# Optimization experiments

Measured on AMD Instinct MI355X. Metric: run time of the kernel, lower is better.

## Reference

```python
import math
import jax, jax.numpy as jnp
import numpy as np

B, S, D, H = 4, 2048, 1024, 16
DK = D // H


def setup_inputs() -> dict:
    key = jax.random.key(0)
    ks = jax.random.split(key, 12)
    scale = 1.0 / math.sqrt(D)
    inp = {
        "query": jax.random.normal(ks[0], (B, S, D), jnp.float32),
        "key": jax.random.normal(ks[1], (B, S, D), jnp.float32),
        "value": jax.random.normal(ks[2], (B, S, D), jnp.float32),
        # causal mask, broadcasts over batch and (after unsqueeze) heads
        "mask": jnp.tril(jnp.ones((1, S, S), jnp.int32)),
        # torch Linear weights: [out_features, in_features]
        "Wq": jax.random.uniform(ks[3], (D, D), jnp.float32, -scale, scale),
        "bq": jax.random.uniform(ks[4], (D,), jnp.float32, -scale, scale),
        "Wk": jax.random.uniform(ks[5], (D, D), jnp.float32, -scale, scale),
        "bk": jax.random.uniform(ks[6], (D,), jnp.float32, -scale, scale),
        "Wv": jax.random.uniform(ks[7], (D, D), jnp.float32, -scale, scale),
        "bv": jax.random.uniform(ks[8], (D,), jnp.float32, -scale, scale),
        "Wo": jax.random.uniform(ks[9], (D, D), jnp.float32, -scale, scale),
        "bo": jax.random.uniform(ks[10], (D,), jnp.float32, -scale, scale),
    }
    return inp


def _proj(x, W, b):
    # torch Linear: x @ W.T + b, then split heads -> [B, H, S, DK]
    y = jnp.einsum('bsd,ed->bse', x, W) + b
    return y.reshape(x.shape[0], x.shape[1], H, DK).transpose(0, 2, 1, 3)


def reference(query, key, value, mask, Wq, bq, Wk, bk, Wv, bv, Wo, bo):
    q = _proj(query, Wq, bq)
    k = _proj(key, Wk, bk)
    v = _proj(value, Wv, bv)
    # scores: [B, H, S, S]
    scores = jnp.einsum('bhqd,bhkd->bhqk', q, k) / math.sqrt(DK)
    m = mask[:, None, :, :]  # mask.unsqueeze(1) -> broadcast over heads
    scores = jnp.where(m == 0, jnp.float32(-1e9), scores)
    prob = jax.nn.softmax(scores, axis=-1)
    # dropout is identity in eval mode
    x = jnp.einsum('bhqk,bhkd->bhqd', prob, v)
    x = x.transpose(0, 2, 1, 3).reshape(query.shape[0], -1, H * DK)
    return jnp.einsum('bsd,ed->bse', x, Wo) + bo
```

## Files before the change

### kernel.cpp

```cpp
#include <hip/hip_runtime.h>
#include <hip/hip_bf16.h>

#define DI __device__ __forceinline__

typedef __bf16 bf16x8 __attribute__((ext_vector_type(8)));
typedef unsigned short u16x8 __attribute__((ext_vector_type(8)));
typedef unsigned short u16x4 __attribute__((ext_vector_type(4)));
typedef unsigned int u32x4 __attribute__((ext_vector_type(4)));
typedef float f32x4 __attribute__((ext_vector_type(4)));
typedef float f32x16 __attribute__((ext_vector_type(16)));

constexpr int kB = 4, kS = 2048, kD = 1024, kH = 16;
constexpr int kM = kB * kS;

DI unsigned short f2bf(float f) {
  union { float f; unsigned u; } x; x.f = f;
  unsigned r = x.u + 0x7fffu + ((x.u >> 16) & 1u);
  return (unsigned short)(r >> 16);
}

DI f32x4 mfma16(u16x8 a, u16x8 b, f32x4 c) {
  return __builtin_amdgcn_mfma_f32_16x16x32_bf16(
      __builtin_bit_cast(bf16x8, a), __builtin_bit_cast(bf16x8, b), c, 0, 0, 0);
}
DI f32x16 mfma32(u16x8 a, u16x8 b, f32x16 c) {
  return __builtin_amdgcn_mfma_f32_32x32x16_bf16(
      __builtin_bit_cast(bf16x8, a), __builtin_bit_cast(bf16x8, b), c, 0, 0, 0);
}

DI void gload16(const unsigned short* g, unsigned short* l) {
  __builtin_amdgcn_global_load_lds(
      (__attribute__((address_space(1))) void*)g,
      (__attribute__((address_space(3))) void*)l, 16, 0, 0);
}

DI unsigned pkbf(float lo, float hi) {
  unsigned r;
  asm("v_cvt_pk_bf16_f32 %0, %1, %2" : "=v"(r) : "v"(lo), "v"(hi));
  return r;
}

__global__ __launch_bounds__(256) void conv_w(const float* __restrict__ s0,
                                              const float* __restrict__ s1,
                                              const float* __restrict__ s2,
                                              const float* __restrict__ s3,
                                              unsigned short* __restrict__ d) {
  const int j = blockIdx.y;
  const float* s = j == 0 ? s0 : j == 1 ? s1 : j == 2 ? s2 : s3;
  const size_t i = ((size_t)blockIdx.x * 256 + threadIdx.x) * 8;
  f32x4 a = *reinterpret_cast<const f32x4*>(s + i);
  f32x4 b = *reinterpret_cast<const f32x4*>(s + i + 4);
  u16x8 o;
#pragma unroll
  for (int jj = 0; jj < 4; ++jj) { o[jj] = f2bf(a[jj]); o[jj + 4] = f2bf(b[jj]); }
  *reinterpret_cast<u16x8*>(d + (size_t)j * 1048576 + i) = o;
}

__global__ __launch_bounds__(256) void proj_gemm(
    const float* __restrict__ A, const unsigned short* __restrict__ W,
    const float* __restrict__ bias, float scale, int vmode,
    unsigned short* __restrict__ O) {
  constexpr int K = kD, N = kD;
  __shared__ unsigned short As[128][64];
  __shared__ unsigned short Bs[2][128][64];

  const int lin = blockIdx.y * 8 + blockIdx.x;
  const int rm = (lin & 7) * 64 + (lin >> 3);
  const int n0 = (rm & 7) * 128, m0 = (rm >> 3) * 128;

  const int t = threadIdx.x;
  const int wave = t >> 6, lane = t & 63;
  const int wr = (wave >> 1) * 64, wc = (wave & 1) * 64;
  const int lrow = lane & 15, lkq = lane >> 4;

  const int rl = lane >> 3;
  const int bcs8 = ((lane & 7) ^ rl) * 8;
  const unsigned short* bsrc = W + ((size_t)(n0 + wave * 32 + rl)) * K + bcs8;
  unsigned short* bl = &Bs[0][0][0] + wave * 2048;

  const int ar_r = t >> 3, ar_c = t & 7;
  const int asw = (ar_c ^ (ar_r & 7)) * 8;
  const float* abase = A + (size_t)(m0 + ar_r) * K + ar_c * 8;

  f32x4 ar0[4], ar1[4];
#pragma unroll
  for (int i = 0; i < 4; ++i) {
    const float* ap = abase + (size_t)i * 32 * K;
    ar0[i] = *reinterpret_cast<const f32x4*>(ap);
    ar1[i] = *reinterpret_cast<const f32x4*>(ap + 4);
  }
#pragma unroll
  for (int i = 0; i < 4; ++i) gload16(bsrc + (size_t)i * 8 * K, bl + i * 512);

  f32x4 acc[4][4];
#pragma unroll
  for (int m = 0; m < 4; ++m)
#pragma unroll
    for (int n = 0; n < 4; ++n) acc[m][n] = f32x4{0.f, 0.f, 0.f, 0.f};

  for (int kt = 0; kt < K; kt += 64) {
    const int cb = (kt >> 6) & 1;
    __builtin_amdgcn_s_barrier();
#pragma unroll
    for (int i = 0; i < 4; ++i) {
      u32x4 w;
      w[0] = pkbf(ar0[i][0], ar0[i][1]);
      w[1] = pkbf(ar0[i][2], ar0[i][3]);
      w[2] = pkbf(ar1[i][0], ar1[i][1]);
      w[3] = pkbf(ar1[i][2], ar1[i][3]);
      *reinterpret_cast<u32x4*>(&As[ar_r + i * 32][asw]) = w;
    }
    asm volatile("s_waitcnt lgkmcnt(0)" ::: "memory");
    __builtin_amdgcn_s_barrier();

    if (kt + 64 < K) {
#pragma unroll
      for (int i = 0; i < 4; ++i)
        gload16(bsrc + (size_t)i * 8 * K + kt + 64, bl + (cb ^ 1) * 8192 + i * 512);
#pragma unroll
      for (int i = 0; i < 4; ++i) {
        const float* ap = abase + (size_t)i * 32 * K + kt + 64;
        ar0[i] = *reinterpret_cast<const f32x4*>(ap);
        ar1[i] = *reinterpret_cast<const f32x4*>(ap + 4);
      }
      asm volatile("s_waitcnt vmcnt(12)" ::: "memory");
    } else {
      asm volatile("s_waitcnt vmcnt(0)" ::: "memory");
    }

    u16x8 af[4][2], bf[4][2];
#pragma unroll
    for (int m = 0; m < 4; ++m) {
      const int row = wr + m * 16 + lrow;
#pragma unroll
      for (int kk = 0; kk < 2; ++kk)
        af[m][kk] = *reinterpret_cast<const u16x8*>(
            &As[row][((kk * 4 + lkq) ^ (row & 7)) * 8]);
    }
#pragma unroll
    for (int n = 0; n < 4; ++n) {
      const int row = wc + n * 16 + lrow;
#pragma unroll
      for (int kk = 0; kk < 2; ++kk)
        bf[n][kk] = *reinterpret_cast<const u16x8*>(
            &Bs[cb][row][((kk * 4 + lkq) ^ (row & 7)) * 8]);
    }
#pragma unroll
    for (int kk = 0; kk < 2; ++kk)
#pragma unroll
      for (int m = 0; m < 4; ++m)
#pragma unroll
        for (int n = 0; n < 4; ++n)
          acc[m][n] = mfma16(af[m][kk], bf[n][kk], acc[m][n]);
  }

#pragma unroll
  for (int n = 0; n < 4; ++n) {
    const int gc = n0 + wc + n * 16 + lrow;
    const float bvv = bias[gc];
#pragma unroll
    for (int m = 0; m < 4; ++m) {
      const int gr = m0 + wr + m * 16 + lkq * 4;
      if (vmode) {
        u16x4 o4;
#pragma unroll
        for (int j = 0; j < 4; ++j) o4[j] = f2bf(acc[m][n][j] + bvv);
        const size_t idx = ((size_t)(gr >> 11) * 1024 + gc) * 2048 + (gr & 2047);
        *reinterpret_cast<u16x4*>(O + idx) = o4;
      } else {
#pragma unroll
        for (int j = 0; j < 4; ++j)
          O[(size_t)(gr + j) * N + gc] = f2bf((acc[m][n][j] + bvv) * scale);
      }
    }
  }
}

__global__ __launch_bounds__(256) void gemm_o(const unsigned short* __restrict__ A,
                                              const unsigned short* __restrict__ W,
                                              const float* __restrict__ bias,
                                              float* __restrict__ C) {
  constexpr int K = kD, N = kD;
  __shared__ unsigned short As[2][128][64];
  __shared__ unsigned short Bs[2][128][64];

  const int lin = blockIdx.y * 8 + blockIdx.x;
  const int rm = (lin & 7) * 64 + (lin >> 3);
  const int n0 = (rm & 7) * 128, m0 = (rm >> 3) * 128;

  const int t = threadIdx.x;
  const int wave = t >> 6, lane = t & 63;
  const int wr = (wave >> 1) * 64, wc = (wave & 1) * 64;
  const int lrow = lane & 15, lkq = lane >> 4;

  const int rl = lane >> 3;
  const int cs8 = ((lane & 7) ^ rl) * 8;
  const unsigned short* asrc = A + ((size_t)(m0 + wave * 32 + rl)) * K + cs8;
  const unsigned short* bsrc = W + ((size_t)(n0 + wave * 32 + rl)) * K + cs8;

#define STAGEO(ii)                                                          \
  {                                                                         \
    const int i_ = (ii);                                                    \
    const int kt_ = i_ * 64;                                                \
    unsigned short* al_ = &As[i_ & 1][0][0] + wave * 2048;                  \
    unsigned short* bl_ = &Bs[i_ & 1][0][0] + wave * 2048;                  \
    _Pragma("unroll") for (int g_ = 0; g_ < 4; ++g_) {                      \
      gload16(asrc + (size_t)g_ * 8 * K + kt_, al_ + g_ * 512);             \
      gload16(bsrc + (size_t)g_ * 8 * K + kt_, bl_ + g_ * 512);             \
    }                                                                       \
  }

  STAGEO(0);

  f32x4 acc[4][4];
#pragma unroll
  for (int m = 0; m < 4; ++m)
#pragma unroll
    for (int n = 0; n < 4; ++n) acc[m][n] = f32x4{0.f, 0.f, 0.f, 0.f};

  for (int i = 0; i < 16; ++i) {
    __builtin_amdgcn_s_barrier();
    if (i + 1 < 16) {
      STAGEO(i + 1);
      asm volatile("s_waitcnt vmcnt(8)" ::: "memory");
    } else {
      asm volatile("s_waitcnt vmcnt(0)" ::: "memory");
    }
    const int cb = i & 1;
    u16x8 af[4][2], bf[4][2];
#pragma unroll
    for (int m = 0; m < 4; ++m) {
      const int row = wr + m * 16 + lrow;
#pragma unroll
      for (int kk = 0; kk < 2; ++kk)
        af[m][kk] = *reinterpret_cast<const u16x8*>(
            &As[cb][row][((kk * 4 + lkq) ^ (row & 7)) * 8]);
    }
#pragma unroll
    for (int n = 0; n < 4; ++n) {
      const int row = wc + n * 16 + lrow;
#pragma unroll
      for (int kk = 0; kk < 2; ++kk)
        bf[n][kk] = *reinterpret_cast<const u16x8*>(
            &Bs[cb][row][((kk * 4 + lkq) ^ (row & 7)) * 8]);
    }
#pragma unroll
    for (int kk = 0; kk < 2; ++kk)
#pragma unroll
      for (int m = 0; m < 4; ++m)
#pragma unroll
        for (int n = 0; n < 4; ++n)
          acc[m][n] = mfma16(af[m][kk], bf[n][kk], acc[m][n]);
  }
#undef STAGEO

#pragma unroll
  for (int n = 0; n < 4; ++n) {
    const int gc = n0 + wc + n * 16 + lrow;
    const float bvv = bias[gc];
#pragma unroll
    for (int m = 0; m < 4; ++m) {
      const int gr = m0 + wr + m * 16 + lkq * 4;
#pragma unroll
      for (int j = 0; j < 4; ++j)
        C[(size_t)(gr + j) * N + gc] = acc[m][n][j] + bvv;
    }
  }
}

__global__ __launch_bounds__(256) void attn_fused(
    const unsigned short* __restrict__ qb, const unsigned short* __restrict__ kb,
    const unsigned short* __restrict__ vbT, unsigned short* __restrict__ ob) {
  __shared__ unsigned short Ks[2][128][64];
  __shared__ unsigned short Vt[2][64][128];

  const int lin = blockIdx.y * 8 + blockIdx.x;
  const int rmap = (lin & 7) * 64 + (lin >> 3);
  const int bh = rmap >> 3;
  const int p = rmap & 7;
  const int b = bh >> 4, h = bh & 15;

  const int t = threadIdx.x;
  const int wave = t >> 6, lane = t & 63;
  const int lq = lane & 31, hi = lane >> 5;
  const int sw7 = lq & 7, sw15 = lq & 15;

  const int np0 = p + 1;
  constexpr int NT = 17;

  const int krl = lane >> 3;
  const int kcs = ((lane & 7) ^ krl) * 8;
  const unsigned short* kbase =
      kb + ((size_t)(b * kS) + wave * 32 + krl) * kD + h * 64 + kcs;
  const int vrl = lane >> 4, vc = lane & 15;
  const size_t vrow = (size_t)(bh * 64) + wave * 16 + vrl;
  const unsigned short* vsrc0 = vbT + (vrow + 0) * kS + (size_t)((vc ^ (vrl + 0)) * 8);
  const unsigned short* vsrc1 = vbT + (vrow + 4) * kS + (size_t)((vc ^ (vrl + 4)) * 8);
  const unsigned short* vsrc2 = vbT + (vrow + 8) * kS + (size_t)((vc ^ (vrl + 8)) * 8);
  const unsigned short* vsrc3 = vbT + (vrow + 12) * kS + (size_t)((vc ^ (vrl + 12)) * 8);

#define STAGE(ii)                                                  \
  {                                                                \
    const int i_ = (ii);                                           \
    const int kv_ = (i_ < np0 ? i_ : i_ - np0) * 128;              \
    unsigned short* kd_ = &Ks[i_ & 1][wave * 32][0];               \
    const unsigned short* kp_ = kbase + (size_t)kv_ * kD;          \
    gload16(kp_, kd_);                                             \
    gload16(kp_ + (size_t)8 * kD, kd_ + 512);                      \
    gload16(kp_ + (size_t)16 * kD, kd_ + 1024);                    \
    gload16(kp_ + (size_t)24 * kD, kd_ + 1536);                    \
    unsigned short* vd_ = &Vt[i_ & 1][wave * 16][0];               \
    gload16(vsrc0 + kv_, vd_);                                     \
    gload16(vsrc1 + kv_, vd_ + 512);                               \
    gload16(vsrc2 + kv_, vd_ + 1024);                              \
    gload16(vsrc3 + kv_, vd_ + 1536);                              \
  }

  int qt = p;
  int qw0 = qt * 128 + wave * 32;
  int qg = qw0 + lq;

  u16x8 bq[4];
  {
    const unsigned short* qrow = qb + ((size_t)(b * kS) + qg) * kD + h * 64;
#pragma unroll
    for (int s = 0; s < 4; ++s)
      bq[s] = *reinterpret_cast<const u16x8*>(qrow + s * 16 + hi * 8);
  }

  f32x16 oT0, oT1;
#pragma unroll
  for (int jj = 0; jj < 16; ++jj) { oT0[jj] = 0.f; oT1[jj] = 0.f; }
  float lsum = 0.f;

  STAGE(0);

  for (int i = 0; i < NT; ++i) {
    if (i == np0) {
      float ls = lsum + __shfl_xor(lsum, 32);
      const float rinv = 1.f / ls;
      unsigned short* orow = ob + ((size_t)(b * kS) + qg) * kD + h * 64 + 4 * hi;
#pragma unroll
      for (int d = 0; d < 2; ++d) {
        const f32x16& oo = d ? oT1 : oT0;
#pragma unroll
        for (int g = 0; g < 4; ++g) {
          u16x4 o4;
#pragma unroll
          for (int jj = 0; jj < 4; ++jj) o4[jj] = f2bf(oo[g * 4 + jj] * rinv);
          *reinterpret_cast<u16x4*>(orow + d * 32 + g * 8) = o4;
        }
      }
      qt = 15 - p;
      qw0 = qt * 128 + wave * 32;
      qg = qw0 + lq;
      const unsigned short* qrow = qb + ((size_t)(b * kS) + qg) * kD + h * 64;
#pragma unroll
      for (int s = 0; s < 4; ++s)
        bq[s] = *reinterpret_cast<const u16x8*>(qrow + s * 16 + hi * 8);
#pragma unroll
      for (int jj = 0; jj < 16; ++jj) { oT0[jj] = 0.f; oT1[jj] = 0.f; }
      lsum = 0.f;
    }

    __builtin_amdgcn_s_barrier();
    if (i + 1 < NT) {
      STAGE(i + 1);
      asm volatile("s_waitcnt vmcnt(8)" ::: "memory");
    } else {
      asm volatile("s_waitcnt vmcnt(0)" ::: "memory");
    }

    const int k0 = (i < np0 ? i : i - np0) * 128;
    if (k0 <= qw0 + 31) {
      const unsigned short* Kc = &Ks[i & 1][0][0];
      const unsigned short* Vc = &Vt[i & 1][0][0];

#pragma unroll
      for (int c = 0; c < 4; ++c) {
        const int k0q = k0 + 32 * c;
        if (k0q > qw0 + 31) continue;

        f32x16 stq;
#pragma unroll
        for (int jj = 0; jj < 16; ++jj) stq[jj] = 0.f;
        __builtin_amdgcn_s_setprio(1);
#pragma unroll
        for (int s = 0; s < 4; ++s) {
          u16x8 ka = *reinterpret_cast<const u16x8*>(
              Kc + (32 * c + lq) * 64 + (((2 * s + hi) ^ sw7) * 8));
          stq = mfma32(ka, bq[s], stq);
        }
        __builtin_amdgcn_s_setprio(0);

        if (k0q + 31 <= qw0) {
#pragma unroll
          for (int r = 0; r < 16; ++r) {
            const float e = exp2f(stq[r]);
            stq[r] = e;
            lsum += e;
          }
        } else {
#pragma unroll
          for (int r = 0; r < 16; ++r) {
            const int kvl = (r & 3) + 8 * (r >> 2) + 4 * hi;
            const float e = (k0q + kvl > qg) ? 0.f : exp2f(stq[r]);
            stq[r] = e;
            lsum += e;
          }
        }

        __builtin_amdgcn_s_setprio(1);
#pragma unroll
        for (int h2 = 0; h2 < 2; ++h2) {
          const int r0 = h2 * 8;
          unsigned P0 = pkbf(stq[r0 + 0], stq[r0 + 1]);
          unsigned P1 = pkbf(stq[r0 + 2], stq[r0 + 3]);
          unsigned P2 = pkbf(stq[r0 + 4], stq[r0 + 5]);
          unsigned P3 = pkbf(stq[r0 + 6], stq[r0 + 7]);
          auto r02 = __builtin_amdgcn_permlane32_swap(P0, P2, false, false);
          auto r13 = __builtin_amdgcn_permlane32_swap(P1, P3, false, false);
          u32x4 w; w[0] = r02[0]; w[1] = r13[0]; w[2] = r02[1]; w[3] = r13[1];
          const u16x8 pf = __builtin_bit_cast(u16x8, w);
          const int ch = ((2 * (2 * c + h2) + hi) ^ sw15) * 8;
          u16x8 va0 = *reinterpret_cast<const u16x8*>(Vc + lq * 128 + ch);
          u16x8 va1 = *reinterpret_cast<const u16x8*>(Vc + (32 + lq) * 128 + ch);
          oT0 = mfma32(va0, pf, oT0);
          oT1 = mfma32(va1, pf, oT1);
        }
        __builtin_amdgcn_s_setprio(0);
      }
    }
  }
#undef STAGE

  float ls = lsum + __shfl_xor(lsum, 32);
  const float rinv = 1.f / ls;
  unsigned short* orow = ob + ((size_t)(b * kS) + qg) * kD + h * 64 + 4 * hi;
#pragma unroll
  for (int d = 0; d < 2; ++d) {
    const f32x16& oo = d ? oT1 : oT0;
#pragma unroll
    for (int g = 0; g < 4; ++g) {
      u16x4 o4;
#pragma unroll
      for (int jj = 0; jj < 4; ++jj) o4[jj] = f2bf(oo[g * 4 + jj] * rinv);
      *reinterpret_cast<u16x4*>(orow + d * 32 + g * 8) = o4;
    }
  }
}

extern "C" void kernel_launch(void* const* d_in, const int* in_sizes, int n_in,
                              void* d_out, int out_size, void* d_ws, size_t ws_size,
                              hipStream_t stream) {
  (void)in_sizes; (void)n_in; (void)out_size; (void)ws_size;
  const float* query = (const float*)d_in[0];
  const float* key_ = (const float*)d_in[1];
  const float* value = (const float*)d_in[2];
  const float* Wq = (const float*)d_in[4];
  const float* bq = (const float*)d_in[5];
  const float* Wk = (const float*)d_in[6];
  const float* bk = (const float*)d_in[7];
  const float* Wv = (const float*)d_in[8];
  const float* bv = (const float*)d_in[9];
  const float* Wo = (const float*)d_in[10];
  const float* bo = (const float*)d_in[11];

  unsigned short* buf0 = (unsigned short*)d_ws;
  unsigned short* wcv = buf0 + (size_t)8 * 1024 * 1024;
  unsigned short* qbuf = wcv + (size_t)4 * 1024 * 1024;
  unsigned short* kbuf = qbuf + (size_t)8 * 1024 * 1024;
  unsigned short* vbT = kbuf + (size_t)8 * 1024 * 1024;

  constexpr float SCL2 = 0.18033688011112042f;

  dim3 gblk(8, 64);
  conv_w<<<dim3(512, 4), 256, 0, stream>>>(Wq, Wk, Wv, Wo, wcv);
  proj_gemm<<<gblk, 256, 0, stream>>>(query, wcv, bq, SCL2, 0, qbuf);
  proj_gemm<<<gblk, 256, 0, stream>>>(key_, wcv + 1048576, bk, 1.f, 0, kbuf);
  proj_gemm<<<gblk, 256, 0, stream>>>(value, wcv + 2 * 1048576, bv, 1.f, 1, vbT);
  attn_fused<<<gblk, 256, 0, stream>>>(qbuf, kbuf, vbT, buf0);
  gemm_o<<<gblk, 256, 0, stream>>>(buf0, wcv + 3 * 1048576, bo, (float*)d_out);
}
```

Before: 178.1 us.

## Split attention into one query tile per block and read V directly from global

The attention kernel stops pairing two query tiles (p and 15-p) in one block and launches one block per 128-row query tile, doubling the grid to 1024 blocks with a swizzled mapping that interleaves long and short causal tiles. V is no longer staged through shared memory; each lane loads its V fragments straight from the transposed global buffer, which halves LDS use and allows four blocks per CU via launch bounds. The K pipeline now waits for all loads at the end of each iteration instead of keeping one stage in flight. The aim is better occupancy and load balance, at the cost of uncoalesced, unshared V global reads and less latency hiding on K.

```diff
diff --git a/kernel.cpp b/kernel.cpp
--- a/kernel.cpp
+++ b/kernel.cpp
@@ -268,174 +268,134 @@
   }
 }
 
-__global__ __launch_bounds__(256) void attn_fused(
+__global__ __launch_bounds__(256, 4) void attn_fused(
     const unsigned short* __restrict__ qb, const unsigned short* __restrict__ kb,
     const unsigned short* __restrict__ vbT, unsigned short* __restrict__ ob) {
   __shared__ unsigned short Ks[2][128][64];
-  __shared__ unsigned short Vt[2][64][128];
-
-  const int lin = blockIdx.y * 8 + blockIdx.x;
-  const int rmap = (lin & 7) * 64 + (lin >> 3);
-  const int bh = rmap >> 3;
-  const int p = rmap & 7;
+
+  const int lin = blockIdx.y * 16 + blockIdx.x;
+  const int xc = lin & 7;
+  const int kk = lin >> 3;
+  const int bh = 8 * xc + (kk >> 4);
+  const int idx = kk & 15;
+  const int j16 = idx ^ (((kk >> 5) & 1) << 3);
+  const int qt = (j16 < 8) ? (15 - j16) : (j16 - 8);
   const int b = bh >> 4, h = bh & 15;
 
   const int t = threadIdx.x;
   const int wave = t >> 6, lane = t & 63;
   const int lq = lane & 31, hi = lane >> 5;
-  const int sw7 = lq & 7, sw15 = lq & 15;
-
-  const int np0 = p + 1;
-  constexpr int NT = 17;
+  const int sw7 = lq & 7;
+
+  const int qw0 = qt * 128 + wave * 32;
+  const int qg = qw0 + lq;
+  const int NT = qt + 1;
 
   const int krl = lane >> 3;
   const int kcs = ((lane & 7) ^ krl) * 8;
   const unsigned short* kbase =
       kb + ((size_t)(b * kS) + wave * 32 + krl) * kD + h * 64 + kcs;
-  const int vrl = lane >> 4, vc = lane & 15;
-  const size_t vrow = (size_t)(bh * 64) + wave * 16 + vrl;
-  const unsigned short* vsrc0 = vbT + (vrow + 0) * kS + (size_t)((vc ^ (vrl + 0)) * 8);
-  const unsigned short* vsrc1 = vbT + (vrow + 4) * kS + (size_t)((vc ^ (vrl + 4)) * 8);
-  const unsigned short* vsrc2 = vbT + (vrow + 8) * kS + (size_t)((vc ^ (vrl + 8)) * 8);
-  const unsigned short* vsrc3 = vbT + (vrow + 12) * kS + (size_t)((vc ^ (vrl + 12)) * 8);
+
+  const unsigned short* vrow0 = vbT + ((size_t)(bh * 64) + lq) * kS + 8 * hi;
+  const unsigned short* vrow1 = vrow0 + (size_t)32 * kS;
+
+  u16x8 bq[4];
+  {
+    const unsigned short* qrow = qb + ((size_t)(b * kS) + qg) * kD + h * 64;
+#pragma unroll
+    for (int s = 0; s < 4; ++s)
+      bq[s] = *reinterpret_cast<const u16x8*>(qrow + s * 16 + hi * 8);
+  }
+
+  f32x16 oT0, oT1;
+#pragma unroll
+  for (int jj = 0; jj < 16; ++jj) { oT0[jj] = 0.f; oT1[jj] = 0.f; }
+  float lsum = 0.f;
 
 #define STAGE(ii)                                                  \
   {                                                                \
     const int i_ = (ii);                                           \
-    const int kv_ = (i_ < np0 ? i_ : i_ - np0) * 128;              \
     unsigned short* kd_ = &Ks[i_ & 1][wave * 32][0];               \
-    const unsigned short* kp_ = kbase + (size_t)kv_ * kD;          \
+    const unsigned short* kp_ = kbase + (size_t)i_ * 128 * kD;     \
     gload16(kp_, kd_);                                             \
     gload16(kp_ + (size_t)8 * kD, kd_ + 512);                      \
     gload16(kp_ + (size_t)16 * kD, kd_ + 1024);                    \
     gload16(kp_ + (size_t)24 * kD, kd_ + 1536);                    \
-    unsigned short* vd_ = &Vt[i_ & 1][wave * 16][0];               \
-    gload16(vsrc0 + kv_, vd_);                                     \
-    gload16(vsrc1 + kv_, vd_ + 512);                               \
-    gload16(vsrc2 + kv_, vd_ + 1024);                              \
-    gload16(vsrc3 + kv_, vd_ + 1536);                              \
-  }
-
-  int qt = p;
-  int qw0 = qt * 128 + wave * 32;
-  int qg = qw0 + lq;
-
-  u16x8 bq[4];
-  {
-    const unsigned short* qrow = qb + ((size_t)(b * kS) + qg) * kD + h * 64;
-#pragma unroll
-    for (int s = 0; s < 4; ++s)
-      bq[s] = *reinterpret_cast<const u16x8*>(qrow + s * 16 + hi * 8);
-  }
-
-  f32x16 oT0, oT1;
-#pragma unroll
-  for (int jj = 0; jj < 16; ++jj) { oT0[jj] = 0.f; oT1[jj] = 0.f; }
-  float lsum = 0.f;
+  }
 
   STAGE(0);
+  asm volatile("s_waitcnt vmcnt(0)" ::: "memory");
+  __builtin_amdgcn_s_barrier();
 
   for (int i = 0; i < NT; ++i) {
-    if (i == np0) {
-      float ls = lsum + __shfl_xor(lsum, 32);
-      const float rinv = 1.f / ls;
-      unsigned short* orow = ob + ((size_t)(b * kS) + qg) * kD + h * 64 + 4 * hi;
-#pragma unroll
-      for (int d = 0; d < 2; ++d) {
-        const f32x16& oo = d ? oT1 : oT0;
-#pragma unroll
-        for (int g = 0; g < 4; ++g) {
-          u16x4 o4;
-#pragma unroll
-          for (int jj = 0; jj < 4; ++jj) o4[jj] = f2bf(oo[g * 4 + jj] * rinv);
-          *reinterpret_cast<u16x4*>(orow + d * 32 + g * 8) = o4;
+    if (i + 1 < NT) STAGE(i + 1);
+    const int k0 = i * 128;
+    const unsigned short* Kc = &Ks[i & 1][0][0];
+
+#pragma unroll
+    for (int c = 0; c < 4; ++c) {
+      const int k0q = k0 + 32 * c;
+      if (k0q > qw0 + 31) continue;
+
+      const u16x8 vv00 = *reinterpret_cast<const u16x8*>(vrow0 + k0q);
+      const u16x8 vv01 = *reinterpret_cast<const u16x8*>(vrow0 + k0q + 16);
+      const u16x8 vv10 = *reinterpret_cast<const u16x8*>(vrow1 + k0q);
+      const u16x8 vv11 = *reinterpret_cast<const u16x8*>(vrow1 + k0q + 16);
+
+      f32x16 stq;
+#pragma unroll
+      for (int jj = 0; jj < 16; ++jj) stq[jj] = 0.f;
+      __builtin_amdgcn_s_setprio(1);
+#pragma unroll
+      for (int s = 0; s < 4; ++s) {
+        u16x8 ka = *reinterpret_cast<const u16x8*>(
+            Kc + (32 * c + lq) * 64 + (((2 * s + hi) ^ sw7) * 8));
+        stq = mfma32(ka, bq[s], stq);
+      }
+      __builtin_amdgcn_s_setprio(0);
+
+      if (k0q + 31 <= qw0) {
+#pragma unroll
+        for (int r = 0; r < 16; ++r) {
+          const float e = exp2f(stq[r]);
+          stq[r] = e;
+          lsum += e;
+        }
+      } else {
+#pragma unroll
+        for (int r = 0; r < 16; ++r) {
+          const int kvl = (r & 3) + 8 * (r >> 2) + 4 * hi;
+          const float e = (k0q + kvl > qg) ? 0.f : exp2f(stq[r]);
+          stq[r] = e;
+          lsum += e;
         }
       }
-      qt = 15 - p;
-      qw0 = qt * 128 + wave * 32;
-      qg = qw0 + lq;
-      const unsigned short* qrow = qb + ((size_t)(b * kS) + qg) * kD + h * 64;
-#pragma unroll
-      for (int s = 0; s < 4; ++s)
-        bq[s] = *reinterpret_cast<const u16x8*>(qrow + s * 16 + hi * 8);
-#pragma unroll
-      for (int jj = 0; jj < 16; ++jj) { oT0[jj] = 0.f; oT1[jj] = 0.f; }
-      lsum = 0.f;
-    }
-
+
+      __builtin_amdgcn_s_setprio(1);
+#pragma unroll
+      for (int h2 = 0; h2 < 2; ++h2) {
+        const int r0 = h2 * 8;
+        unsigned P0 = pkbf(stq[r0 + 0], stq[r0 + 1]);
+        unsigned P1 = pkbf(stq[r0 + 2], stq[r0 + 3]);
+        unsigned P2 = pkbf(stq[r0 + 4], stq[r0 + 5]);
+        unsigned P3 = pkbf(stq[r0 + 6], stq[r0 + 7]);
+        auto r02 = __builtin_amdgcn_permlane32_swap(P0, P2, false, false);
+        auto r13 = __builtin_amdgcn_permlane32_swap(P1, P3, false, false);
+        u32x4 w; w[0] = r02[0]; w[1] = r13[0]; w[2] = r02[1]; w[3] = r13[1];
+        const u16x8 pf = __builtin_bit_cast(u16x8, w);
+        oT0 = mfma32(h2 ? vv01 : vv00, pf, oT0);
+        oT1 = mfma32(h2 ? vv11 : vv10, pf, oT1);
+      }
+      __builtin_amdgcn_s_setprio(0);
+    }
+
+    asm volatile("s_waitcnt vmcnt(0)" ::: "memory");
     __builtin_amdgcn_s_barrier();
-    if (i + 1 < NT) {
-      STAGE(i + 1);
-      asm volatile("s_waitcnt vmcnt(8)" ::: "memory");
-    } else {
-      asm volatile("s_waitcnt vmcnt(0)" ::: "memory");
-    }
-
-    const int k0 = (i < np0 ? i : i - np0) * 128;
-    if (k0 <= qw0 + 31) {
-      const unsigned short* Kc = &Ks[i & 1][0][0];
-      const unsigned short* Vc = &Vt[i & 1][0][0];
-
-#pragma unroll
-      for (int c = 0; c < 4; ++c) {
-        const int k0q = k0 + 32 * c;
-        if (k0q > qw0 + 31) continue;
-
-        f32x16 stq;
-#pragma unroll
-        for (int jj = 0; jj < 16; ++jj) stq[jj] = 0.f;
-        __builtin_amdgcn_s_setprio(1);
-#pragma unroll
-        for (int s = 0; s < 4; ++s) {
-          u16x8 ka = *reinterpret_cast<const u16x8*>(
-              Kc + (32 * c + lq) * 64 + (((2 * s + hi) ^ sw7) * 8));
-          stq = mfma32(ka, bq[s], stq);
-        }
-        __builtin_amdgcn_s_setprio(0);
-
-        if (k0q + 31 <= qw0) {
-#pragma unroll
-          for (int r = 0; r < 16; ++r) {
-            const float e = exp2f(stq[r]);
-            stq[r] = e;
-            lsum += e;
-          }
-        } else {
-#pragma unroll
-          for (int r = 0; r < 16; ++r) {
-            const int kvl = (r & 3) + 8 * (r >> 2) + 4 * hi;
-            const float e = (k0q + kvl > qg) ? 0.f : exp2f(stq[r]);
-            stq[r] = e;
-            lsum += e;
-          }
-        }
-
-        __builtin_amdgcn_s_setprio(1);
-#pragma unroll
-        for (int h2 = 0; h2 < 2; ++h2) {
-          const int r0 = h2 * 8;
-          unsigned P0 = pkbf(stq[r0 + 0], stq[r0 + 1]);
-          unsigned P1 = pkbf(stq[r0 + 2], stq[r0 + 3]);
-          unsigned P2 = pkbf(stq[r0 + 4], stq[r0 + 5]);
-          unsigned P3 = pkbf(stq[r0 + 6], stq[r0 + 7]);
-          auto r02 = __builtin_amdgcn_permlane32_swap(P0, P2, false, false);
-          auto r13 = __builtin_amdgcn_permlane32_swap(P1, P3, false, false);
-          u32x4 w; w[0] = r02[0]; w[1] = r13[0]; w[2] = r02[1]; w[3] = r13[1];
-          const u16x8 pf = __builtin_bit_cast(u16x8, w);
-          const int ch = ((2 * (2 * c + h2) + hi) ^ sw15) * 8;
-          u16x8 va0 = *reinterpret_cast<const u16x8*>(Vc + lq * 128 + ch);
-          u16x8 va1 = *reinterpret_cast<const u16x8*>(Vc + (32 + lq) * 128 + ch);
-          oT0 = mfma32(va0, pf, oT0);
-          oT1 = mfma32(va1, pf, oT1);
-        }
-        __builtin_amdgcn_s_setprio(0);
-      }
-    }
   }
 #undef STAGE
 
-  float ls = lsum + __shfl_xor(lsum, 32);
-  const float rinv = 1.f / ls;
+  lsum += __shfl_xor(lsum, 32);
+  const float rinv = 1.f / lsum;
   unsigned short* orow = ob + ((size_t)(b * kS) + qg) * kD + h * 64 + 4 * hi;
 #pragma unroll
   for (int d = 0; d < 2; ++d) {
@@ -479,6 +439,6 @@
   proj_gemm<<<gblk, 256, 0, stream>>>(query, wcv, bq, SCL2, 0, qbuf);
   proj_gemm<<<gblk, 256, 0, stream>>>(key_, wcv + 1048576, bk, 1.f, 0, kbuf);
   proj_gemm<<<gblk, 256, 0, stream>>>(value, wcv + 2 * 1048576, bv, 1.f, 1, vbT);
-  attn_fused<<<gblk, 256, 0, stream>>>(qbuf, kbuf, vbT, buf0);
+  attn_fused<<<dim3(16, 64), 256, 0, stream>>>(qbuf, kbuf, vbT, buf0);
   gemm_o<<<gblk, 256, 0, stream>>>(buf0, wcv + 3 * 1048576, bo, (float*)d_out);
 }
```

Measured after the change: 197.5 us. 10.9% more time.
